# Optimization experiments

Measured on AMD Instinct MI355X. Metric: run time of the kernel, lower is better.

## Reference

```python
import jax, jax.numpy as jnp
import numpy as np

QK_K = 256          # values per Q4_K super-block
TYPE_SIZE = 144     # bytes per Q4_K block: 2 (d fp16) + 2 (dmin fp16) + 12 (scales) + 128 (qs)
OUT_FEATURES = 8192
IN_FEATURES = 8192
BATCH = 256


def setup_inputs() -> dict:
    rng = np.random.default_rng(0)
    n_blocks = OUT_FEATURES * IN_FEATURES // QK_K
    # Pack valid little-endian fp16 super-block scales into raw bytes (as a GGUF file would store them).
    d16 = rng.uniform(0.001, 0.01, size=(n_blocks,)).astype(np.float16)
    dmin16 = rng.uniform(0.0005, 0.005, size=(n_blocks,)).astype(np.float16)
    scales = rng.integers(0, 256, size=(n_blocks, 12), dtype=np.uint8)  # packed 6-bit sub-scales/mins
    qs = rng.integers(0, 256, size=(n_blocks, 128), dtype=np.uint8)     # 4-bit quants, 2 per byte
    blocks = np.concatenate(
        [d16.view(np.uint8).reshape(n_blocks, 2),
         dmin16.view(np.uint8).reshape(n_blocks, 2),
         scales, qs], axis=1)  # [n_blocks, 144] uint8
    key = jax.random.key(0)
    kx, kb = jax.random.split(key)
    x = jax.random.normal(kx, (BATCH, IN_FEATURES), dtype=jnp.float32)
    bias = jax.random.normal(kb, (OUT_FEATURES,), dtype=jnp.float32) * 0.01
    return {"x": x, "qweight": jnp.asarray(blocks), "bias": bias}


def _bitcast_f16(bytes2):
    # bytes2: [n, 2] uint8 (little-endian) -> [n] float32
    n = bytes2.shape[0]
    return jax.lax.bitcast_convert_type(bytes2.reshape(n, 1, 2), jnp.float16).reshape(n).astype(jnp.float32)


def _get_scale_min(scales):
    # scales: [n, 12] uint8 -> 8 six-bit sub-block scales and mins, each [n, 8]
    n = scales.shape[0]
    s = scales.reshape(n, 3, 4)
    d_, m_, md = s[:, 0], s[:, 1], s[:, 2]  # each [n, 4]
    sc = jnp.concatenate([d_ & 63, (md & 15) | ((d_ >> 2) & 48)], axis=-1)
    mn = jnp.concatenate([m_ & 63, (md >> 4) | ((m_ >> 2) & 48)], axis=-1)
    return sc, mn


def dequantize_q4_k(blocks):
    # blocks: [n_blocks, 144] uint8 -> [n_blocks, 256] float32
    n = blocks.shape[0]
    d = _bitcast_f16(blocks[:, 0:2])       # [n]
    dmin = _bitcast_f16(blocks[:, 2:4])    # [n]
    sc, mn = _get_scale_min(blocks[:, 4:16])
    dl = (d[:, None] * sc.astype(jnp.float32)).reshape(n, 8, 1)   # per-sub-block scale
    ml = (dmin[:, None] * mn.astype(jnp.float32)).reshape(n, 8, 1)  # per-sub-block min
    qs = blocks[:, 16:].reshape(n, 4, 1, 32)                       # 128 bytes
    shift = jnp.array([0, 4], dtype=jnp.uint8).reshape(1, 1, 2, 1)
    q = ((qs >> shift) & 15).reshape(n, 8, 32).astype(jnp.float32)  # low then high nibbles
    return (dl * q - ml).reshape(n, QK_K)


def reference(x, qweight, bias):
    qweight = qweight.astype(jnp.uint8)
    W = dequantize_q4_k(qweight).reshape(OUT_FEATURES, IN_FEATURES)  # [out, in]
    return x @ W.T + bias  # F.linear(x, W, bias)
```

## Files before the change

### kernel.cpp

```cpp
#include <hip/hip_runtime.h>
#include <hip/hip_fp16.h>

typedef __bf16 bf16x8 __attribute__((ext_vector_type(8)));
typedef float floatx16 __attribute__((ext_vector_type(16)));
typedef unsigned int uint;
typedef unsigned short ushort;
typedef uint  uintx4  __attribute__((ext_vector_type(4)));
typedef float floatx4 __attribute__((ext_vector_type(4)));

constexpr int Mdim = 256, Ndim = 8192, Kdim = 8192;
constexpr int BN = 64, KSPLIT = 4;
constexpr int KS = Kdim / KSPLIT;
constexpr int NT = KS / 64;
constexpr int KB = Kdim / 256;

union U8 { uint u[4]; bf16x8 v; };

__device__ __forceinline__ uint cvtpk(float lo, float hi) {
  uint r; asm("v_cvt_pk_bf16_f32 %0, %1, %2" : "=v"(r) : "v"(lo), "v"(hi));
  return r;
}

template <typename T>
__device__ __forceinline__ T gld(const void* p) {
  return *(const __attribute__((address_space(1))) T*)p;
}

__device__ __forceinline__ int bswz(int row, int ch) {
  return row * 128 + ((ch ^ (row & 15)) << 3);
}

template<bool PRE, bool PART>
__global__ __launch_bounds__(256, 2)
void q4k_gemm(const float* __restrict__ x, const bf16x8* __restrict__ xbf,
              const int* __restrict__ qw, const float* __restrict__ bias,
              float* __restrict__ out, float* __restrict__ pout)
{
  __shared__ ushort Bb[2][BN * 128];

  const int tid = threadIdx.x;
  const int bid = blockIdx.x;
  const int l  = (bid & 7) * 64 + (bid >> 3);
  const int nb = l >> 2;
  const int ks = l & 3;
  const int n0 = nb * BN;
  const int ks8 = ks * (KS >> 8);

  const int sr = tid >> 2;
  const int sq = tid & 3;

  const int lane = tid & 63;
  const int wave = tid >> 6;
  const int mb0  = wave * 2;
  const int brow = lane & 31;
  const int bco  = lane >> 5;

  const int* bp0 = qw + (n0 + sr) * (KB * 144);
  const bf16x8* xA0 = PRE ? (xbf + ((mb0    ) * 512 + ks * 128) * 64 + lane) : nullptr;
  const bf16x8* xA1 = PRE ? (xbf + ((mb0 + 1) * 512 + ks * 128) * 64 + lane) : nullptr;

  uintx4 R[4][2];
  uintx4 Mdd[2], M0[2], M1[2], M2[2];
  U8 pqL, pqH;
  bf16x8 aA[8], aB[8];
  floatx16 acc00 = {}, acc01 = {}, acc10 = {}, acc11 = {};

  auto gloadB = [&](int s2, int rs) {
    const int* qp = bp0 + (ks8 + (s2 >> 2)) * 144 + 16 + (s2 & 3) * 32 + sq * 8;
    R[rs][0] = gld<uintx4>(qp);
    R[rs][1] = gld<uintx4>(qp + 4);
  };

  auto mload = [&](int sbrel, int ms) {
    const int* bp = bp0 + (ks8 + sbrel) * 144;
    Mdd[ms] = gld<uintx4>(bp);
    M0[ms]  = gld<uintx4>(bp + 4);
    M1[ms]  = gld<uintx4>(bp + 8);
    M2[ms]  = gld<uintx4>(bp + 12);
  };

  auto gloadA = [&](int t, bf16x8 (&A)[8]) {
    if constexpr (PRE) {
      const int f = t * 4 * 64;
      #pragma unroll
      for (int kk = 0; kk < 4; ++kk) {
        A[kk]     = gld<bf16x8>(xA0 + f + kk * 64);
        A[4 + kk] = gld<bf16x8>(xA1 + f + kk * 64);
      }
    } else {
      const int kg = ks * KS + t * 64 + bco * 8;
      #pragma unroll
      for (int kk = 0; kk < 4; ++kk) {
        const float* fA = x + (mb0 * 32 + brow) * Kdim + kg + kk * 16;
        const float* fB = x + ((mb0 + 1) * 32 + brow) * Kdim + kg + kk * 16;
        const floatx4 p0 = gld<floatx4>(fA), p1 = gld<floatx4>(fA + 4);
        const floatx4 q0 = gld<floatx4>(fB), q1 = gld<floatx4>(fB + 4);
        U8 ua, ub;
        ua.u[0] = cvtpk(p0.x, p0.y); ua.u[1] = cvtpk(p0.z, p0.w);
        ua.u[2] = cvtpk(p1.x, p1.y); ua.u[3] = cvtpk(p1.z, p1.w);
        ub.u[0] = cvtpk(q0.x, q0.y); ub.u[1] = cvtpk(q0.z, q0.w);
        ub.u[2] = cvtpk(q1.x, q1.y); ub.u[3] = cvtpk(q1.z, q1.w);
        A[kk] = ua.v; A[4 + kk] = ub.v;
      }
    }
  };

  auto dequant = [&](int c, int rs, int ms) {
    const uintx4 dd = Mdd[ms];
    const float d  = __half2float(__ushort_as_half((ushort)((dd.x & 255u) | ((dd.y & 255u) << 8))));
    const float dm = __half2float(__ushort_as_half((ushort)((dd.z & 255u) | ((dd.w & 255u) << 8))));
    const uintx4 s0 = M0[ms], s1 = M1[ms], s2 = M2[ms];
    uint scA, scB, mnA, mnB;
    if (c == 0)      { scA = s0.x & 63u; scB = s0.y & 63u; mnA = s1.x & 63u; mnB = s1.y & 63u; }
    else if (c == 1) { scA = s0.z & 63u; scB = s0.w & 63u; mnA = s1.z & 63u; mnB = s1.w & 63u; }
    else if (c == 2) {
      scA = (s2.x & 15u) | ((s0.x >> 2) & 48u); scB = (s2.y & 15u) | ((s0.y >> 2) & 48u);
      mnA = (s2.x >> 4)  | ((s1.x >> 2) & 48u); mnB = (s2.y >> 4)  | ((s1.y >> 2) & 48u);
    } else {
      scA = (s2.z & 15u) | ((s0.z >> 2) & 48u); scB = (s2.w & 15u) | ((s0.w >> 2) & 48u);
      mnA = (s2.z >> 4)  | ((s1.z >> 2) & 48u); mnB = (s2.w >> 4)  | ((s1.w >> 2) & 48u);
    }
    const float dlA = d * (float)scA, mlA = dm * (float)mnA;
    const float dlB = d * (float)scB, mlB = dm * (float)mnB;
    float wl[8], wh[8];
    #pragma unroll
    for (int h = 0; h < 2; ++h) {
      const uintx4 qv = R[rs][h];
      wl[h*4+0] = fmaf(dlA, (float)(qv.x & 15u), -mlA);
      wl[h*4+1] = fmaf(dlA, (float)(qv.y & 15u), -mlA);
      wl[h*4+2] = fmaf(dlA, (float)(qv.z & 15u), -mlA);
      wl[h*4+3] = fmaf(dlA, (float)(qv.w & 15u), -mlA);
      wh[h*4+0] = fmaf(dlB, (float)(qv.x >> 4), -mlB);
      wh[h*4+1] = fmaf(dlB, (float)(qv.y >> 4), -mlB);
      wh[h*4+2] = fmaf(dlB, (float)(qv.z >> 4), -mlB);
      wh[h*4+3] = fmaf(dlB, (float)(qv.w >> 4), -mlB);
    }
    #pragma unroll
    for (int p = 0; p < 4; ++p) {
      pqL.u[p] = cvtpk(wl[2*p], wl[2*p+1]);
      pqH.u[p] = cvtpk(wh[2*p], wh[2*p+1]);
    }
  };

  auto bwrite = [&](int bufi, int h) {
    *(bf16x8*)&Bb[bufi][bswz(sr, h * 8 + sq)]     = pqL.v;
    *(bf16x8*)&Bb[bufi][bswz(sr, h * 8 + 4 + sq)] = pqH.v;
  };

  auto mstep = [&](int bufi, int h, const bf16x8 (&A)[8]) {
    #pragma unroll
    for (int kk = 0; kk < 4; ++kk) {
      const bf16x8 bq0 = *(const bf16x8*)&Bb[bufi][bswz(brow,      h * 8 + kk * 2 + bco)];
      const bf16x8 bq1 = *(const bf16x8*)&Bb[bufi][bswz(brow + 32, h * 8 + kk * 2 + bco)];
      acc00 = __builtin_amdgcn_mfma_f32_32x32x16_bf16(A[kk],     bq0, acc00, 0, 0, 0);
      acc01 = __builtin_amdgcn_mfma_f32_32x32x16_bf16(A[kk],     bq1, acc01, 0, 0, 0);
      acc10 = __builtin_amdgcn_mfma_f32_32x32x16_bf16(A[4 + kk], bq0, acc10, 0, 0, 0);
      acc11 = __builtin_amdgcn_mfma_f32_32x32x16_bf16(A[4 + kk], bq1, acc11, 0, 0, 0);
    }
  };

  mload(0, 0); mload(1, 1);
  gloadB(0, 0); gloadB(1, 1); gloadB(2, 2); gloadB(3, 3);
  gloadA(0, aA); gloadA(1, aB);
  dequant(0, 0, 0); bwrite(0, 0);
  dequant(1, 1, 0); bwrite(0, 1);
  asm volatile("s_waitcnt lgkmcnt(0)" ::: "memory");
  __builtin_amdgcn_s_barrier();
  __builtin_amdgcn_sched_barrier(0);

  #define MLOADJ(j)                                                          \
    if ((j) == 1) { const int sb_ = B / 2 + 2; if (sb_ < 8) mload(sb_, 0); } \
    else if ((j) == 3) { const int sb_ = B / 2 + 3; if (sb_ < 8) mload(sb_, 1); }

  #define PH2(j) {                                                           \
    const int p_ = B + (j);                                                  \
    const int s1_ = 2 * p_ + 2, s2_ = 2 * p_ + 3;                            \
    if (s1_ < NT) { dequant((2*(j)+2)&3, (2*(j)+2)&3, (((j)+1)>>1)&1);       \
                    bwrite(((j)&1)^1, 0); }                                  \
    if (s2_ < NT) { dequant((2*(j)+3)&3, (2*(j)+3)&3, (((j)+1)>>1)&1);       \
                    bwrite(((j)&1)^1, 1); }                                  \
    if (s1_ + 2 < NT) gloadB(s1_ + 2, (2*(j)+4)&3);                          \
    if (s2_ + 2 < NT) gloadB(s2_ + 2, (2*(j)+5)&3);                          \
    MLOADJ(j)                                                                \
    __builtin_amdgcn_s_setprio(1);                                           \
    mstep((j)&1, 0, aA);                                                     \
    __builtin_amdgcn_s_setprio(0);                                           \
    if (s1_ < NT) gloadA(s1_, aA);                                           \
    __builtin_amdgcn_s_setprio(1);                                           \
    mstep((j)&1, 1, aB);                                                     \
    __builtin_amdgcn_s_setprio(0);                                           \
    if (s2_ < NT) gloadA(s2_, aB);                                           \
    asm volatile("s_waitcnt lgkmcnt(0)" ::: "memory");                       \
    __builtin_amdgcn_s_barrier();                                            \
    __builtin_amdgcn_sched_barrier(0);                                       \
  }

  for (int i = 0; i < 4; ++i) {
    const int B = i * 4;
    PH2(0) PH2(1) PH2(2) PH2(3)
  }
  #undef PH2
  #undef MLOADJ

  const int gn0 = n0 + (lane & 31);
  const int gn1 = gn0 + 32;
  const int mrow = wave * 64 + 4 * (lane >> 5);
  if constexpr (PART) {
    float* pp = pout + (size_t)ks * ((size_t)Mdim * Ndim);
    #pragma unroll
    for (int r = 0; r < 16; ++r) {
      const int m = mrow + (r & 3) + 8 * (r >> 2);
      pp[m * Ndim + gn0] = acc00[r];
      pp[m * Ndim + gn1] = acc01[r];
      pp[(m + 32) * Ndim + gn0] = acc10[r];
      pp[(m + 32) * Ndim + gn1] = acc11[r];
    }
  } else {
    const float bv0 = (ks == 0) ? bias[gn0] : 0.0f;
    const float bv1 = (ks == 0) ? bias[gn1] : 0.0f;
    #pragma unroll
    for (int r = 0; r < 16; ++r) {
      const int m = mrow + (r & 3) + 8 * (r >> 2);
      atomicAdd(&out[m * Ndim + gn0], acc00[r] + bv0);
      atomicAdd(&out[m * Ndim + gn1], acc01[r] + bv1);
      atomicAdd(&out[(m + 32) * Ndim + gn0], acc10[r] + bv0);
      atomicAdd(&out[(m + 32) * Ndim + gn1], acc11[r] + bv1);
    }
  }
}

__global__ __launch_bounds__(256)
void reduce4(const floatx4* __restrict__ p, const float* __restrict__ bias,
             floatx4* __restrict__ out)
{
  const int gid = blockIdx.x * 256 + threadIdx.x;
  constexpr int STR = (Mdim * Ndim) / 4;
  floatx4 s = gld<floatx4>(p + gid);
  s += gld<floatx4>(p + gid + STR);
  s += gld<floatx4>(p + gid + 2 * STR);
  s += gld<floatx4>(p + gid + 3 * STR);
  s += gld<floatx4>((const floatx4*)bias + (gid & 2047));
  out[gid] = s;
}

template<bool DOCVT, bool ZERO>
__global__ __launch_bounds__(256)
void prep(const float* __restrict__ x, uintx4* __restrict__ xb,
          floatx4* __restrict__ out)
{
  const int gid = blockIdx.x * 256 + threadIdx.x;
  if (ZERO) {
    out[gid * 2]     = floatx4{0.f, 0.f, 0.f, 0.f};
    out[gid * 2 + 1] = floatx4{0.f, 0.f, 0.f, 0.f};
  }
  if (DOCVT) {
    const int lane = gid & 63;
    const int m = ((gid >> 15) * 32) + (lane & 31);
    const int k = (((gid >> 6) & 511) * 16) + (lane >> 5) * 8;
    const floatx4 f0 = gld<floatx4>(x + m * Kdim + k);
    const floatx4 f1 = gld<floatx4>(x + m * Kdim + k + 4);
    uintx4 st;
    st.x = cvtpk(f0.x, f0.y); st.y = cvtpk(f0.z, f0.w);
    st.z = cvtpk(f1.x, f1.y); st.w = cvtpk(f1.z, f1.w);
    xb[gid] = st;
  }
}

extern "C" void kernel_launch(void* const* d_in, const int* in_sizes, int n_in,
                              void* d_out, int out_size, void* d_ws, size_t ws_size,
                              hipStream_t stream) {
  (void)in_sizes; (void)n_in; (void)out_size;
  const float* x    = (const float*)d_in[0];
  const int*   qw   = (const int*)d_in[1];
  const float* bias = (const float*)d_in[2];
  float* out = (float*)d_out;

  const size_t needXB   = (size_t)Mdim * Kdim * 2;
  const size_t needPART = needXB + (size_t)KSPLIT * Mdim * Ndim * 4;
  if (ws_size >= needPART) {
    float* part = (float*)((char*)d_ws + needXB);
    prep<true, false><<<1024, 256, 0, stream>>>(x, (uintx4*)d_ws, (floatx4*)out);
    q4k_gemm<true, true><<<512, 256, 0, stream>>>(
        x, (const bf16x8*)d_ws, qw, bias, out, part);
    reduce4<<<(Mdim * Ndim / 4) / 256, 256, 0, stream>>>(
        (const floatx4*)part, bias, (floatx4*)out);
  } else if (ws_size >= needXB) {
    prep<true, true><<<1024, 256, 0, stream>>>(x, (uintx4*)d_ws, (floatx4*)out);
    q4k_gemm<true, false><<<512, 256, 0, stream>>>(
        x, (const bf16x8*)d_ws, qw, bias, out, nullptr);
  } else {
    prep<false, true><<<1024, 256, 0, stream>>>(x, nullptr, (floatx4*)out);
    q4k_gemm<false, false><<<512, 256, 0, stream>>>(
        x, nullptr, qw, bias, out, nullptr);
  }
}
```

Measured before the change: 61.40 us.

## Stage Q4_K quants via global_load_lds ring and single-step pipeline

Replaces the register-held quant prefetch with direct global-to-LDS loads into a six-slot swizzled ring, and restructures the main loop into one 32-step unrolled pipeline with a half-size B tile per step. Explicit vmcnt waits govern how far loads run ahead. The aim is to free the VGPRs that held prefetched quants and to deepen prefetch, so more memory latency overlaps with the MFMA work. In exchange it uses more LDS, adds an LDS read per dequant, and depends on hand-tuned vmcnt counts that must match the exact number of outstanding loads.

```diff
diff --git a/kernel.cpp b/kernel.cpp
--- a/kernel.cpp
+++ b/kernel.cpp
@@ -20,15 +20,20 @@
   uint r; asm("v_cvt_pk_bf16_f32 %0, %1, %2" : "=v"(r) : "v"(lo), "v"(hi));
   return r;
 }
-
 template <typename T>
 __device__ __forceinline__ T gld(const void* p) {
   return *(const __attribute__((address_space(1))) T*)p;
 }
-
+__device__ __forceinline__ void glds16(const void* g, void* l) {
+  __builtin_amdgcn_global_load_lds(
+      (const __attribute__((address_space(1))) uint*)g,
+      (__attribute__((address_space(3))) uint*)l, 16, 0, 0);
+}
 __device__ __forceinline__ int bswz(int row, int ch) {
-  return row * 128 + ((ch ^ (row & 15)) << 3);
-}
+  return row * 64 + ((ch ^ (row & 7)) << 3);
+}
+#define WAITVM_(n) asm volatile("s_waitcnt vmcnt(" #n ")" ::: "memory")
+#define WAITVM(n) WAITVM_(n)
 
 template<bool PRE, bool PART>
 __global__ __launch_bounds__(256, 2)
@@ -36,7 +41,8 @@
               const int* __restrict__ qw, const float* __restrict__ bias,
               float* __restrict__ out, float* __restrict__ pout)
 {
-  __shared__ ushort Bb[2][BN * 128];
+  __shared__ __align__(16) int Qs[6 * 2048];
+  __shared__ ushort Bb[2][BN * 64];
 
   const int tid = threadIdx.x;
   const int bid = blockIdx.x;
@@ -59,16 +65,21 @@
   const bf16x8* xA0 = PRE ? (xbf + ((mb0    ) * 512 + ks * 128) * 64 + lane) : nullptr;
   const bf16x8* xA1 = PRE ? (xbf + ((mb0 + 1) * 512 + ks * 128) * 64 + lane) : nullptr;
 
-  uintx4 R[4][2];
   uintx4 Mdd[2], M0[2], M1[2], M2[2];
   U8 pqL, pqH;
-  bf16x8 aA[8], aB[8];
+  bf16x8 aE[8], aO[8];
   floatx16 acc00 = {}, acc01 = {}, acc10 = {}, acc11 = {};
 
-  auto gloadB = [&](int s2, int rs) {
-    const int* qp = bp0 + (ks8 + (s2 >> 2)) * 144 + 16 + (s2 & 3) * 32 + sq * 8;
-    R[rs][0] = gld<uintx4>(qp);
-    R[rs][1] = gld<uintx4>(qp + 4);
+  auto stageQ = [&](int s, int slot) {
+    const int sb = s >> 2, c64 = s & 3;
+    const int schk = ((lane & 7) ^ (lane >> 3)) << 2;
+    #pragma unroll
+    for (int j = 0; j < 2; ++j) {
+      const int r = j * 32 + wave * 8 + (lane >> 3);
+      const int* src = qw + (n0 + r) * (KB * 144) + (ks8 + sb) * 144
+                       + 16 + c64 * 32 + schk;
+      glds16((const void*)src, (void*)&Qs[slot * 2048 + (j * 256 + wave * 64) * 4]);
+    }
   };
 
   auto mload = [&](int sbrel, int ms) {
@@ -105,7 +116,10 @@
     }
   };
 
-  auto dequant = [&](int c, int rs, int ms) {
+  auto dequant = [&](int c, int slot, int ms) {
+    const int* qrow = &Qs[slot * 2048 + sr * 32];
+    const uintx4 q0 = *(const uintx4*)(qrow + (((2 * sq)     ^ (sr & 7)) << 2));
+    const uintx4 q1 = *(const uintx4*)(qrow + (((2 * sq + 1) ^ (sr & 7)) << 2));
     const uintx4 dd = Mdd[ms];
     const float d  = __half2float(__ushort_as_half((ushort)((dd.x & 255u) | ((dd.y & 255u) << 8))));
     const float dm = __half2float(__ushort_as_half((ushort)((dd.z & 255u) | ((dd.w & 255u) << 8))));
@@ -125,7 +139,7 @@
     float wl[8], wh[8];
     #pragma unroll
     for (int h = 0; h < 2; ++h) {
-      const uintx4 qv = R[rs][h];
+      const uintx4 qv = h ? q1 : q0;
       wl[h*4+0] = fmaf(dlA, (float)(qv.x & 15u), -mlA);
       wl[h*4+1] = fmaf(dlA, (float)(qv.y & 15u), -mlA);
       wl[h*4+2] = fmaf(dlA, (float)(qv.z & 15u), -mlA);
@@ -142,16 +156,16 @@
     }
   };
 
-  auto bwrite = [&](int bufi, int h) {
-    *(bf16x8*)&Bb[bufi][bswz(sr, h * 8 + sq)]     = pqL.v;
-    *(bf16x8*)&Bb[bufi][bswz(sr, h * 8 + 4 + sq)] = pqH.v;
-  };
-
-  auto mstep = [&](int bufi, int h, const bf16x8 (&A)[8]) {
+  auto bwrite = [&](int bufi) {
+    *(bf16x8*)&Bb[bufi][bswz(sr, sq)]     = pqL.v;
+    *(bf16x8*)&Bb[bufi][bswz(sr, 4 + sq)] = pqH.v;
+  };
+
+  auto mstep = [&](int bufi, const bf16x8 (&A)[8]) {
     #pragma unroll
     for (int kk = 0; kk < 4; ++kk) {
-      const bf16x8 bq0 = *(const bf16x8*)&Bb[bufi][bswz(brow,      h * 8 + kk * 2 + bco)];
-      const bf16x8 bq1 = *(const bf16x8*)&Bb[bufi][bswz(brow + 32, h * 8 + kk * 2 + bco)];
+      const bf16x8 bq0 = *(const bf16x8*)&Bb[bufi][bswz(brow,      kk * 2 + bco)];
+      const bf16x8 bq1 = *(const bf16x8*)&Bb[bufi][bswz(brow + 32, kk * 2 + bco)];
       acc00 = __builtin_amdgcn_mfma_f32_32x32x16_bf16(A[kk],     bq0, acc00, 0, 0, 0);
       acc01 = __builtin_amdgcn_mfma_f32_32x32x16_bf16(A[kk],     bq1, acc01, 0, 0, 0);
       acc10 = __builtin_amdgcn_mfma_f32_32x32x16_bf16(A[4 + kk], bq0, acc10, 0, 0, 0);
@@ -159,48 +173,53 @@
     }
   };
 
+  stageQ(0, 0); stageQ(1, 1); stageQ(2, 2); stageQ(3, 3);
+  gloadA(0, aE);
   mload(0, 0); mload(1, 1);
-  gloadB(0, 0); gloadB(1, 1); gloadB(2, 2); gloadB(3, 3);
-  gloadA(0, aA); gloadA(1, aB);
-  dequant(0, 0, 0); bwrite(0, 0);
-  dequant(1, 1, 0); bwrite(0, 1);
+  WAITVM(20);
+  __builtin_amdgcn_s_barrier();
+  dequant(0, 0, 0);
+  bwrite(0);
   asm volatile("s_waitcnt lgkmcnt(0)" ::: "memory");
   __builtin_amdgcn_s_barrier();
   __builtin_amdgcn_sched_barrier(0);
 
-  #define MLOADJ(j)                                                          \
-    if ((j) == 1) { const int sb_ = B / 2 + 2; if (sb_ < 8) mload(sb_, 0); } \
-    else if ((j) == 3) { const int sb_ = B / 2 + 3; if (sb_ < 8) mload(sb_, 1); }
-
-  #define PH2(j) {                                                           \
-    const int p_ = B + (j);                                                  \
-    const int s1_ = 2 * p_ + 2, s2_ = 2 * p_ + 3;                            \
-    if (s1_ < NT) { dequant((2*(j)+2)&3, (2*(j)+2)&3, (((j)+1)>>1)&1);       \
-                    bwrite(((j)&1)^1, 0); }                                  \
-    if (s2_ < NT) { dequant((2*(j)+3)&3, (2*(j)+3)&3, (((j)+1)>>1)&1);       \
-                    bwrite(((j)&1)^1, 1); }                                  \
-    if (s1_ + 2 < NT) gloadB(s1_ + 2, (2*(j)+4)&3);                          \
-    if (s2_ + 2 < NT) gloadB(s2_ + 2, (2*(j)+5)&3);                          \
-    MLOADJ(j)                                                                \
+  #define PH(P, CA, NA, NVM) {                                               \
+    if ((P) + 1 < NT) gloadA((P) + 1, NA);                                   \
+    if ((P) + 4 < NT) stageQ((P) + 4, ((P) + 4) % 6);                        \
+    if ((P) % 4 == 3 && ((P) + 5) / 4 <= 7)                                  \
+      mload(((P) + 5) / 4, (((P) + 5) / 4) & 1);                             \
+    __builtin_amdgcn_sched_barrier(0);                                       \
+    if ((P) + 1 < NT) {                                                      \
+      dequant(((P) + 1) & 3, ((P) + 1) % 6, (((P) + 1) >> 2) & 1);           \
+      bwrite(((P) + 1) & 1);                                                 \
+    }                                                                        \
     __builtin_amdgcn_s_setprio(1);                                           \
-    mstep((j)&1, 0, aA);                                                     \
+    mstep((P) & 1, CA);                                                      \
     __builtin_amdgcn_s_setprio(0);                                           \
-    if (s1_ < NT) gloadA(s1_, aA);                                           \
-    __builtin_amdgcn_s_setprio(1);                                           \
-    mstep((j)&1, 1, aB);                                                     \
-    __builtin_amdgcn_s_setprio(0);                                           \
-    if (s2_ < NT) gloadA(s2_, aB);                                           \
+    NVM;                                                                     \
     asm volatile("s_waitcnt lgkmcnt(0)" ::: "memory");                       \
     __builtin_amdgcn_s_barrier();                                            \
     __builtin_amdgcn_sched_barrier(0);                                       \
   }
 
-  for (int i = 0; i < 4; ++i) {
-    const int B = i * 4;
-    PH2(0) PH2(1) PH2(2) PH2(3)
-  }
-  #undef PH2
-  #undef MLOADJ
+  PH(0,  aE, aO, WAITVM(20)) PH(1,  aO, aE, WAITVM(20))
+  PH(2,  aE, aO, WAITVM(20)) PH(3,  aO, aE, WAITVM(20))
+  PH(4,  aE, aO, WAITVM(20)) PH(5,  aO, aE, WAITVM(20))
+  PH(6,  aE, aO, WAITVM(20)) PH(7,  aO, aE, WAITVM(20))
+  PH(8,  aE, aO, WAITVM(20)) PH(9,  aO, aE, WAITVM(20))
+  PH(10, aE, aO, WAITVM(20)) PH(11, aO, aE, WAITVM(20))
+  PH(12, aE, aO, WAITVM(20)) PH(13, aO, aE, WAITVM(20))
+  PH(14, aE, aO, WAITVM(20)) PH(15, aO, aE, WAITVM(20))
+  PH(16, aE, aO, WAITVM(20)) PH(17, aO, aE, WAITVM(20))
+  PH(18, aE, aO, WAITVM(20)) PH(19, aO, aE, WAITVM(20))
+  PH(20, aE, aO, WAITVM(20)) PH(21, aO, aE, WAITVM(20))
+  PH(22, aE, aO, WAITVM(20)) PH(23, aO, aE, WAITVM(20))
+  PH(24, aE, aO, WAITVM(20)) PH(25, aO, aE, WAITVM(20))
+  PH(26, aE, aO, WAITVM(20)) PH(27, aO, aE, WAITVM(20))
+  PH(28, aE, aO, WAITVM(16)) PH(29, aO, aE, WAITVM(12))
+  PH(30, aE, aO, (void)0)    PH(31, aO, aE, (void)0)
+  #undef PH
 
   const int gn0 = n0 + (lane & 31);
   const int gn1 = gn0 + 32;
```

Result: slower. 67.41 us (+9.8%).
